# Kernel tuning notes

Hardware: AMD Instinct MI355X
Metric: run time of the kernel (lower is better)

Reference implementation:

```python
import jax, jax.numpy as jnp
import numpy as np

N_NODES = 50000
N_EDGES = 800000
D_IN = 128
D_HID = 128
N_CLASSES = 40


def gcn_conv(h, src, dst, W, b, n_nodes):
    """GCNConv: out = D^{-1/2} (A + I) D^{-1/2} (h @ W) + b, with self-loops."""
    h = h @ W  # [N, F_out]
    loop = jnp.arange(n_nodes, dtype=src.dtype)
    s = jnp.concatenate([src, loop])  # [E + N]
    d = jnp.concatenate([dst, loop])
    deg = jax.ops.segment_sum(jnp.ones_like(d, dtype=h.dtype), d, num_segments=n_nodes)
    dinv = jax.lax.rsqrt(jnp.maximum(deg, 1.0))  # deg >= 1 due to self-loops
    norm = dinv[s] * dinv[d]  # [E + N]
    msgs = h[s] * norm[:, None]  # gather: [E + N, F_out]
    out = jax.ops.segment_sum(msgs, d, num_segments=n_nodes)  # scatter-add
    return out + b


def setup_inputs() -> dict:
    key = jax.random.key(0)
    ks = jax.random.split(key, 12)
    x = jax.random.normal(ks[0], (N_NODES, D_IN), dtype=jnp.float32)
    edge_index = jax.random.randint(ks[1], (2, N_EDGES), 0, N_NODES, dtype=jnp.int64)
    def lin(k, fi, fo):
        s = 1.0 / np.sqrt(fi)
        return jax.random.uniform(k, (fi, fo), jnp.float32, -s, s)
    W_pre = lin(ks[2], D_IN, D_HID)
    b_pre = jnp.zeros((D_HID,), jnp.float32)
    W1 = lin(ks[3], D_HID, D_HID)
    b1 = jnp.zeros((D_HID,), jnp.float32)
    W2 = lin(ks[4], D_HID, D_HID)
    b2 = jnp.zeros((D_HID,), jnp.float32)
    W_post = lin(ks[5], D_HID, N_CLASSES)
    b_post = jnp.zeros((N_CLASSES,), jnp.float32)
    return {"x": x, "edge_index": edge_index, "W_pre": W_pre, "b_pre": b_pre,
            "W1": W1, "b1": b1, "W2": W2, "b2": b2,
            "W_post": W_post, "b_post": b_post}


def reference(x, edge_index, W_pre, b_pre, W1, b1, W2, b2, W_post, b_post):
    src, dst = edge_index[0], edge_index[1]
    n = x.shape[0]
    h = x @ W_pre + b_pre                      # pre-process MLP (Linear)
    h = jax.nn.relu(gcn_conv(h, src, dst, W1, b1, n))   # conv1 + act1
    h = jax.nn.relu(gcn_conv(h, src, dst, W2, b2, n))   # conv2 + act2
    return h @ W_post + b_post                 # post-process MLP (Linear)
```

## Files before the change

kernel.cpp:

```cpp
#include <hip/hip_runtime.h>

#define D 128

typedef short bfrag __attribute__((ext_vector_type(8)));
typedef float f32x4 __attribute__((ext_vector_type(4)));
typedef unsigned uint32;

__device__ inline unsigned short bf16_rne(float x) {
    unsigned u = __float_as_uint(x);
    return (unsigned short)((u + 0x7FFFu + ((u >> 16) & 1u)) >> 16);
}
__device__ inline float bf16_to_f(unsigned short h) {
    return __uint_as_float(((unsigned)h) << 16);
}
__device__ inline unsigned split2p(float x) {
    unsigned short hi = bf16_rne(x);
    unsigned short lo = bf16_rne(x - bf16_to_f(hi));
    return (unsigned)hi | ((unsigned)lo << 16);
}

__device__ inline void unpair_r(uint4 q0, uint4 q1, bfrag& ah, bfrag& al) {
    union { uint32 u[4]; bfrag b; } H, L;
    H.u[0] = __builtin_amdgcn_perm(q0.y, q0.x, 0x05040100u);
    H.u[1] = __builtin_amdgcn_perm(q0.w, q0.z, 0x05040100u);
    H.u[2] = __builtin_amdgcn_perm(q1.y, q1.x, 0x05040100u);
    H.u[3] = __builtin_amdgcn_perm(q1.w, q1.z, 0x05040100u);
    L.u[0] = __builtin_amdgcn_perm(q0.y, q0.x, 0x07060302u);
    L.u[1] = __builtin_amdgcn_perm(q0.w, q0.z, 0x07060302u);
    L.u[2] = __builtin_amdgcn_perm(q1.y, q1.x, 0x07060302u);
    L.u[3] = __builtin_amdgcn_perm(q1.w, q1.z, 0x07060302u);
    ah = H.b;
    al = L.b;
}

__device__ inline void split8_r(uint4 q0, uint4 q1, bfrag& ah, bfrag& al) {
    float v[8] = {__uint_as_float(q0.x), __uint_as_float(q0.y), __uint_as_float(q0.z), __uint_as_float(q0.w),
                  __uint_as_float(q1.x), __uint_as_float(q1.y), __uint_as_float(q1.z), __uint_as_float(q1.w)};
    union { unsigned short us[8]; bfrag b; } H, L;
    #pragma unroll
    for (int i = 0; i < 8; i++) {
        unsigned pr = split2p(v[i]);
        H.us[i] = (unsigned short)pr;
        L.us[i] = (unsigned short)(pr >> 16);
    }
    ah = H.b;
    al = L.b;
}

__global__ __launch_bounds__(256) void deg_raw(const unsigned* __restrict__ raw, int* __restrict__ deg,
                                               int* __restrict__ gmode, int E) {
    __shared__ int smode;
    int p0 = blockIdx.x * 1024;
    if (threadIdx.x < 64) {
        int p = p0 + threadIdx.x * 16;
        unsigned v = (p < E) ? raw[2 * p + 1] : 0u;
        unsigned long long any = __ballot(v != 0u);
        if (threadIdx.x == 0) smode = (any != 0ull) ? 1 : 0;
    }
    __syncthreads();
    int m = smode;
    if (blockIdx.x == 0 && threadIdx.x == 0) *gmode = m;
    int pend = min(p0 + 1024, E);
    for (int p = p0 + threadIdx.x; p < pend; p += 256) {
        int d = m ? (int)raw[E + p] : (int)((const unsigned long long*)raw)[E + p];
        atomicAdd(&deg[d], 1);
    }
}

__global__ __launch_bounds__(256) void rank_block(const int* __restrict__ deg, float* __restrict__ dinv,
                                                  int* __restrict__ local_rank, int* __restrict__ hist_blk, int N) {
    __shared__ int h[256];
    int t = threadIdx.x;
    h[t] = 0;
    __syncthreads();
    int i = blockIdx.x * 256 + t;
    if (i < N) {
        int d = deg[i];
        dinv[i] = 1.0f / sqrtf((float)(d + 1));
        int b = min(d, 255);
        local_rank[i] = atomicAdd(&h[b], 1);
    }
    __syncthreads();
    hist_blk[blockIdx.x * 256 + t] = h[t];
}

__global__ __launch_bounds__(256) void scan_blocks(int* __restrict__ hist_blk, int* __restrict__ binbase,
                                                   int* __restrict__ ebase, int nblk) {
    int b = threadIdx.x;
    int sum = 0;
    int k = 0;
    for (; k + 8 <= nblk; k += 8) {
        int v[8];
        #pragma unroll
        for (int u = 0; u < 8; u++) v[u] = hist_blk[(k + u) * 256 + b];
        #pragma unroll
        for (int u = 0; u < 8; u++) { hist_blk[(k + u) * 256 + b] = sum; sum += v[u]; }
    }
    for (; k < nblk; k++) {
        int v = hist_blk[k * 256 + b];
        hist_blk[k * 256 + b] = sum;
        sum += v;
    }
    __shared__ int s[256], s2[256];
    int c = sum, e = sum * b;
    s[b] = c; s2[b] = e;
    __syncthreads();
    for (int off = 1; off < 256; off <<= 1) {
        int a0 = (b >= off) ? s[b - off] : 0;
        int a1 = (b >= off) ? s2[b - off] : 0;
        __syncthreads();
        s[b] += a0; s2[b] += a1;
        __syncthreads();
    }
    binbase[b] = s[b] - c;
    ebase[b] = s2[b] - e;
}

__global__ __launch_bounds__(256) void emit_perm(const int* __restrict__ deg, const float* __restrict__ dinv,
                                                 const int* __restrict__ local_rank, const int* __restrict__ hist_blk,
                                                 const int* __restrict__ binbase, const int* __restrict__ ebase,
                                                 int* __restrict__ tailcur, int* __restrict__ rowbeg,
                                                 int* __restrict__ cursor, uint4* __restrict__ meta, int N) {
    int i = blockIdx.x * 256 + threadIdx.x;
    if (i >= N) return;
    int d = deg[i];
    int b = min(d, 255);
    int rib = hist_blk[blockIdx.x * 256 + b] + local_rank[i];
    int pos = binbase[b] + rib;
    int rb = (b < 255) ? (ebase[b] + rib * b) : (ebase[255] + atomicAdd(tailcur, d));
    rowbeg[i] = rb;
    cursor[i] = 0;
    meta[pos] = make_uint4((unsigned)rb, (unsigned)d, __float_as_uint(dinv[i]), (unsigned)i);
}

__global__ __launch_bounds__(256) void fill_csr_raw(const unsigned* __restrict__ raw, const int* __restrict__ gmode,
                                                    const int* __restrict__ rowbeg, int* __restrict__ cursor,
                                                    unsigned short* __restrict__ csr16, int E) {
    int e = blockIdx.x * 256 + threadIdx.x;
    if (e >= E) return;
    int m = *gmode;
    int d = m ? (int)raw[E + e] : (int)((const unsigned long long*)raw)[E + e];
    int s = m ? (int)raw[e]     : (int)((const unsigned long long*)raw)[e];
    int pos = atomicAdd(&cursor[d], 1);
    csr16[rowbeg[d] + pos] = (unsigned short)s;
}

__global__ __launch_bounds__(256) void prep_w_all(const float* __restrict__ Wpre, const float* __restrict__ W1,
                                                  const float* __restrict__ W2, const float* __restrict__ Wpost,
                                                  unsigned short* __restrict__ preh, unsigned short* __restrict__ prel,
                                                  unsigned short* __restrict__ w1h, unsigned short* __restrict__ w1l,
                                                  unsigned short* __restrict__ w2h, unsigned short* __restrict__ w2l,
                                                  unsigned short* __restrict__ poh, unsigned short* __restrict__ pol) {
    int i = blockIdx.x * 256 + threadIdx.x;
    const float* W; unsigned short *wh, *wl; int idx, ncols;
    if (i < 16384)      { W = Wpre;  wh = preh; wl = prel; idx = i;         ncols = 128; }
    else if (i < 32768) { W = W1;    wh = w1h;  wl = w1l;  idx = i - 16384; ncols = 128; }
    else if (i < 49152) { W = W2;    wh = w2h;  wl = w2l;  idx = i - 32768; ncols = 128; }
    else if (i < 55296) { W = Wpost; wh = poh;  wl = pol;  idx = i - 49152; ncols = 40;  }
    else return;
    int n = idx >> 7, k = idx & 127;
    float v = (n < ncols) ? W[k * ncols + n] : 0.f;
    unsigned p = split2p(v);
    wh[idx] = (unsigned short)p;
    wl[idx] = (unsigned short)(p >> 16);
}

template<int NTILES, int EPI, int AFMT, int NW>
__global__ __launch_bounds__(NW * 64) void gemm_mfma(const void* __restrict__ Ap,
                                                     const unsigned short* __restrict__ Wth,
                                                     const unsigned short* __restrict__ Wtl,
                                                     const float* __restrict__ bias,
                                                     const float* __restrict__ dinv,
                                                     float* __restrict__ Cf,
                                                     uint32* __restrict__ Pout,
                                                     int nStrips, int N, int outW) {
    int wave = threadIdx.x >> 6;
    int lane = threadIdx.x & 63;
    int l15 = lane & 15, lg = lane >> 4;
    int so, colbase;
    if (NW == 8) { so = wave >> 1; colbase = (wave & 1) * 64; }
    else         { so = wave;      colbase = 0; }
    size_t chunkStride = (size_t)nStrips * 256;

    bfrag wh[4][NTILES], wl[4][NTILES];
    #pragma unroll
    for (int ks = 0; ks < 4; ks++)
        #pragma unroll
        for (int nt = 0; nt < NTILES; nt++) {
            size_t off = (size_t)(colbase + nt * 16 + l15) * D + ks * 32 + lg * 8;
            wh[ks][nt] = *(const bfrag*)(Wth + off);
            wl[ks][nt] = *(const bfrag*)(Wtl + off);
        }

    const int stride = gridDim.x * 4;
    int strip = blockIdx.x * 4 + so;
    if (strip >= nStrips) return;

    uint4 cur[8];
    auto loadraw = [&](int s, uint4* r) {
        int arow = min(s * 16 + l15, N - 1);
        const uint4* p = (const uint4*)Ap + (size_t)arow * 32 + lg * 2;
        #pragma unroll
        for (int ks = 0; ks < 4; ks++) {
            r[2 * ks]     = p[ks * 8];
            r[2 * ks + 1] = p[ks * 8 + 1];
        }
    };

    loadraw(strip, cur);
    while (true) {
        int next = strip + stride;
        bool has_next = next < nStrips;
        uint4 nxt[8];
        if (has_next) loadraw(next, nxt);

        bfrag ah[4], al[4];
        #pragma unroll
        for (int ks = 0; ks < 4; ks++) {
            if (AFMT == 0) unpair_r(cur[2 * ks], cur[2 * ks + 1], ah[ks], al[ks]);
            else           split8_r(cur[2 * ks], cur[2 * ks + 1], ah[ks], al[ks]);
        }
        f32x4 acc[NTILES];
        #pragma unroll
        for (int nt = 0; nt < NTILES; nt++) acc[nt] = (f32x4){0.f, 0.f, 0.f, 0.f};
        #pragma unroll
        for (int ks = 0; ks < 4; ks++) {
            #pragma unroll
            for (int nt = 0; nt < NTILES; nt++)
                acc[nt] = __builtin_amdgcn_mfma_f32_16x16x32_bf16(ah[ks], wh[ks][nt], acc[nt], 0, 0, 0);
            #pragma unroll
            for (int nt = 0; nt < NTILES; nt++)
                acc[nt] = __builtin_amdgcn_mfma_f32_16x16x32_bf16(ah[ks], wl[ks][nt], acc[nt], 0, 0, 0);
            #pragma unroll
            for (int nt = 0; nt < NTILES; nt++)
                acc[nt] = __builtin_amdgcn_mfma_f32_16x16x32_bf16(al[ks], wh[ks][nt], acc[nt], 0, 0, 0);
        }

        int row0 = strip * 16;
        float dv[4];
        if (EPI == 0) {
            #pragma unroll
            for (int r = 0; r < 4; r++) {
                int row = row0 + lg * 4 + r;
                dv[r] = (row < N) ? dinv[row] : 0.f;
            }
        }
        #pragma unroll
        for (int nt = 0; nt < NTILES; nt++) {
            int col = colbase + nt * 16 + l15;
            #pragma unroll
            for (int r = 0; r < 4; r++) {
                int row = row0 + lg * 4 + r;
                if (row >= N) continue;
                float v = acc[nt][r];
                if (EPI == 0) {
                    Cf[(size_t)(col >> 4) * chunkStride + (size_t)row * 16 + (col & 15)] = v * dv[r];
                } else if (EPI == 1) {
                    Pout[(size_t)row * D + col] = split2p(v + bias[col]);
                } else {
                    if (col < outW) Cf[(size_t)row * outW + col] = v + bias[col];
                }
            }
        }
        if (!has_next) break;
        #pragma unroll
        for (int i = 0; i < 8; i++) cur[i] = nxt[i];
        strip = next;
    }
}

__global__ __launch_bounds__(256) void gather_xcd(const unsigned short* __restrict__ csr16,
                                                  const uint4* __restrict__ meta,
                                                  const float* __restrict__ t_c, const float* __restrict__ bias,
                                                  uint32* __restrict__ Pout, int N, int nStrips) {
    int chunk = blockIdx.x & 7;
    int k = (blockIdx.x >> 3) * 16 + (threadIdx.x >> 4);
    if (k >= N) return;
    uint4 m = meta[k];
    int beg = (int)m.x;
    int end = beg + (int)m.y;
    float di = __uint_as_float(m.z);
    int node = (int)m.w;
    int w = (threadIdx.x >> 2) & 3;
    int c = threadIdx.x & 3;
    const float* tc = t_c + (size_t)chunk * nStrips * 256 + c * 4;
    float4 a0 = make_float4(0.f, 0.f, 0.f, 0.f);
    float4 a1 = make_float4(0.f, 0.f, 0.f, 0.f);
    int j = beg + w;
    for (; j + 12 < end; j += 16) {
        int o0 = csr16[j];
        int o1 = csr16[j + 4];
        int o2 = csr16[j + 8];
        int o3 = csr16[j + 12];
        float4 v0 = *(const float4*)(tc + ((size_t)o0 << 4));
        float4 v1 = *(const float4*)(tc + ((size_t)o1 << 4));
        float4 v2 = *(const float4*)(tc + ((size_t)o2 << 4));
        float4 v3 = *(const float4*)(tc + ((size_t)o3 << 4));
        a0.x += v0.x; a0.y += v0.y; a0.z += v0.z; a0.w += v0.w;
        a1.x += v1.x; a1.y += v1.y; a1.z += v1.z; a1.w += v1.w;
        a0.x += v2.x; a0.y += v2.y; a0.z += v2.z; a0.w += v2.w;
        a1.x += v3.x; a1.y += v3.y; a1.z += v3.z; a1.w += v3.w;
    }
    for (; j < end; j += 4) {
        int o0 = csr16[j];
        float4 v0 = *(const float4*)(tc + ((size_t)o0 << 4));
        a0.x += v0.x; a0.y += v0.y; a0.z += v0.z; a0.w += v0.w;
    }
    a0.x += a1.x; a0.y += a1.y; a0.z += a1.z; a0.w += a1.w;
    a0.x += __shfl_xor(a0.x, 4); a0.y += __shfl_xor(a0.y, 4);
    a0.z += __shfl_xor(a0.z, 4); a0.w += __shfl_xor(a0.w, 4);
    a0.x += __shfl_xor(a0.x, 8); a0.y += __shfl_xor(a0.y, 8);
    a0.z += __shfl_xor(a0.z, 8); a0.w += __shfl_xor(a0.w, 8);
    if (w != 0) return;
    float4 tv = *(const float4*)(tc + (size_t)node * 16);
    int col0 = chunk * 16 + c * 4;
    float4 b = *((const float4*)bias + (col0 >> 2));
    float4 r;
    r.x = fmaxf(fmaf(di, a0.x + tv.x, b.x), 0.f);
    r.y = fmaxf(fmaf(di, a0.y + tv.y, b.y), 0.f);
    r.z = fmaxf(fmaf(di, a0.z + tv.z, b.z), 0.f);
    r.w = fmaxf(fmaf(di, a0.w + tv.w, b.w), 0.f);
    uint4 p;
    p.x = split2p(r.x); p.y = split2p(r.y); p.z = split2p(r.z); p.w = split2p(r.w);
    *(uint4*)(Pout + (size_t)node * D + col0) = p;
}

extern "C" void kernel_launch(void* const* d_in, const int* in_sizes, int n_in,
                              void* d_out, int out_size, void* d_ws, size_t ws_size,
                              hipStream_t stream) {
    const float* x      = (const float*)d_in[0];
    const unsigned* edges = (const unsigned*)d_in[1];
    const float* W_pre  = (const float*)d_in[2];
    const float* b_pre  = (const float*)d_in[3];
    const float* W1     = (const float*)d_in[4];
    const float* b1     = (const float*)d_in[5];
    const float* W2     = (const float*)d_in[6];
    const float* b2     = (const float*)d_in[7];
    const float* W_post = (const float*)d_in[8];
    const float* b_post = (const float*)d_in[9];
    float* out = (float*)d_out;

    const int N = in_sizes[0] / D;
    const int E = in_sizes[1] / 2;
    const int nStrips = (N + 15) / 16;
    const int Npad = nStrips * 16;
    const int nBlk = (N + 255) / 256;

    char* ws = (char*)d_ws;
    size_t off = 0;
    auto alloc = [&](size_t bytes) { void* p = ws + off; off += (bytes + 255) & ~(size_t)255; return p; };
    uint32* pairA = (uint32*)alloc((size_t)Npad * D * 4);
    uint32* pairB = (uint32*)alloc((size_t)Npad * D * 4);
    float*  bufT  = (float*)alloc((size_t)Npad * D * 4);
    float*  dinv    = (float*)alloc((size_t)N * 4);
    int*    deg     = (int*)alloc((size_t)N * 4);
    int*    rowbeg  = (int*)alloc((size_t)N * 4);
    unsigned short* csr16 = (unsigned short*)alloc((size_t)E * 2);
    uint4*  meta    = (uint4*)alloc((size_t)N * 16);
    unsigned short* wpre_h  = (unsigned short*)alloc(128 * 128 * 2);
    unsigned short* wpre_l  = (unsigned short*)alloc(128 * 128 * 2);
    unsigned short* w1_h    = (unsigned short*)alloc(128 * 128 * 2);
    unsigned short* w1_l    = (unsigned short*)alloc(128 * 128 * 2);
    unsigned short* w2_h    = (unsigned short*)alloc(128 * 128 * 2);
    unsigned short* w2_l    = (unsigned short*)alloc(128 * 128 * 2);
    unsigned short* wpost_h = (unsigned short*)alloc(48 * 128 * 2);
    unsigned short* wpost_l = (unsigned short*)alloc(48 * 128 * 2);

    {
        char* t = (char*)bufT;
        size_t toff = 0;
        auto talloc = [&](size_t bytes) { void* p = t + toff; toff += (bytes + 255) & ~(size_t)255; return p; };
        int* cursor     = (int*)talloc((size_t)N * 4);
        int* local_rank = (int*)talloc((size_t)N * 4);
        int* hist_blk   = (int*)talloc((size_t)nBlk * 256 * 4);
        int* mode2      = (int*)talloc(256);
        int* binbase    = (int*)talloc(1024);
        int* ebase      = (int*)talloc(1024);
        int* gmode = mode2;
        int* tailcur = mode2 + 1;

        (void)hipMemsetAsync(mode2, 0, 8, stream);
        (void)hipMemsetAsync(deg, 0, (size_t)N * 4, stream);
        deg_raw<<<(E + 1023) / 1024, 256, 0, stream>>>(edges, deg, gmode, E);
        rank_block<<<nBlk, 256, 0, stream>>>(deg, dinv, local_rank, hist_blk, N);
        scan_blocks<<<1, 256, 0, stream>>>(hist_blk, binbase, ebase, nBlk);
        emit_perm<<<nBlk, 256, 0, stream>>>(deg, dinv, local_rank, hist_blk, binbase, ebase,
                                            tailcur, rowbeg, cursor, meta, N);
        fill_csr_raw<<<(E + 255) / 256, 256, 0, stream>>>(edges, gmode, rowbeg, cursor, csr16, E);
    }

    prep_w_all<<<216, 256, 0, stream>>>(W_pre, W1, W2, W_post,
                                        wpre_h, wpre_l, w1_h, w1_l, w2_h, w2_l, wpost_h, wpost_l);

    const int nGatherBlocks = ((N + 15) / 16) * 8;

    gemm_mfma<4, 1, 1, 8><<<196, 512, 0, stream>>>(x, wpre_h, wpre_l, b_pre, nullptr, nullptr, pairB, nStrips, N, D);

    gemm_mfma<4, 0, 0, 8><<<196, 512, 0, stream>>>(pairB, w1_h, w1_l, nullptr, dinv, bufT, nullptr, nStrips, N, D);
    gather_xcd<<<nGatherBlocks, 256, 0, stream>>>(csr16, meta, bufT, b1, pairA, N, nStrips);

    gemm_mfma<4, 0, 0, 8><<<196, 512, 0, stream>>>(pairA, w2_h, w2_l, nullptr, dinv, bufT, nullptr, nStrips, N, D);
    gather_xcd<<<nGatherBlocks, 256, 0, stream>>>(csr16, meta, bufT, b2, pairB, N, nStrips);

    gemm_mfma<3, 2, 0, 4><<<196, 256, 0, stream>>>(pairB, wpost_h, wpost_l, b_post, nullptr, out, nullptr, nStrips, N, 40);
}
```

Baseline: 306.0 us.

## Pad CSR rows to multiples of four with sentinel zero rows for vector gather

Each CSR row's length is rounded up to a multiple of four. Padding slots are filled with a sentinel node index that points at zeroed extra rows appended to each feature chunk. The gather kernel can then load four indices with one ushort4 read, drop its remainder loop, and accumulate into four independent registers. The GEMM grid also grows from 196 to 256 blocks. In exchange the kernel adds sentinel initialisation work, a larger CSR buffer, and some wasted gathers of the zero row.

```diff
diff --git a/kernel.cpp b/kernel.cpp
--- a/kernel.cpp
+++ b/kernel.cpp
@@ -48,8 +48,11 @@
 }
 
 __global__ __launch_bounds__(256) void deg_raw(const unsigned* __restrict__ raw, int* __restrict__ deg,
-                                               int* __restrict__ gmode, int E) {
+                                               int* __restrict__ gmode, unsigned short* __restrict__ csr16,
+                                               float* __restrict__ t_c, int E, int N, int csrCap4, int nRows) {
     __shared__ int smode;
+    int gid = blockIdx.x * 256 + threadIdx.x;
+    int gstride = gridDim.x * 256;
     int p0 = blockIdx.x * 1024;
     if (threadIdx.x < 64) {
         int p = p0 + threadIdx.x * 16;
@@ -60,6 +63,15 @@
     __syncthreads();
     int m = smode;
     if (blockIdx.x == 0 && threadIdx.x == 0) *gmode = m;
+    unsigned short sent = (unsigned short)N;
+    ushort4 s4 = make_ushort4(sent, sent, sent, sent);
+    for (int i = gid; i < csrCap4; i += gstride) ((ushort4*)csr16)[i] = s4;
+    int nSentF4 = 8 * (nRows - N) * 4;
+    for (int i = gid; i < nSentF4; i += gstride) {
+        int chunk = i / ((nRows - N) * 4);
+        int rem = i % ((nRows - N) * 4);
+        ((float4*)(t_c + (size_t)chunk * nRows * 16 + (size_t)N * 16))[rem] = make_float4(0.f, 0.f, 0.f, 0.f);
+    }
     int pend = min(p0 + 1024, E);
     for (int p = p0 + threadIdx.x; p < pend; p += 256) {
         int d = m ? (int)raw[E + p] : (int)((const unsigned long long*)raw)[E + p];
@@ -102,7 +114,8 @@
         sum += v;
     }
     __shared__ int s[256], s2[256];
-    int c = sum, e = sum * b;
+    int bp = (b + 3) & ~3;
+    int c = sum, e = sum * bp;
     s[b] = c; s2[b] = e;
     __syncthreads();
     for (int off = 1; off < 256; off <<= 1) {
@@ -125,12 +138,13 @@
     if (i >= N) return;
     int d = deg[i];
     int b = min(d, 255);
+    int dp = (d + 3) & ~3;
     int rib = hist_blk[blockIdx.x * 256 + b] + local_rank[i];
     int pos = binbase[b] + rib;
-    int rb = (b < 255) ? (ebase[b] + rib * b) : (ebase[255] + atomicAdd(tailcur, d));
+    int rb = (b < 255) ? (ebase[b] + rib * ((b + 3) & ~3)) : (ebase[255] + atomicAdd(tailcur, dp));
     rowbeg[i] = rb;
     cursor[i] = 0;
-    meta[pos] = make_uint4((unsigned)rb, (unsigned)d, __float_as_uint(dinv[i]), (unsigned)i);
+    meta[pos] = make_uint4((unsigned)rb, (unsigned)dp, __float_as_uint(dinv[i]), (unsigned)i);
 }
 
 __global__ __launch_bounds__(256) void fill_csr_raw(const unsigned* __restrict__ raw, const int* __restrict__ gmode,
@@ -173,14 +187,14 @@
                                                      const float* __restrict__ dinv,
                                                      float* __restrict__ Cf,
                                                      uint32* __restrict__ Pout,
-                                                     int nStrips, int N, int outW) {
+                                                     int nStrips, int N, int outW, int nRows) {
     int wave = threadIdx.x >> 6;
     int lane = threadIdx.x & 63;
     int l15 = lane & 15, lg = lane >> 4;
     int so, colbase;
     if (NW == 8) { so = wave >> 1; colbase = (wave & 1) * 64; }
     else         { so = wave;      colbase = 0; }
-    size_t chunkStride = (size_t)nStrips * 256;
+    size_t chunkStride = (size_t)nRows * 16;
 
     bfrag wh[4][NTILES], wl[4][NTILES];
     #pragma unroll
@@ -272,41 +286,37 @@
 __global__ __launch_bounds__(256) void gather_xcd(const unsigned short* __restrict__ csr16,
                                                   const uint4* __restrict__ meta,
                                                   const float* __restrict__ t_c, const float* __restrict__ bias,
-                                                  uint32* __restrict__ Pout, int N, int nStrips) {
+                                                  uint32* __restrict__ Pout, int N, int nRows) {
     int chunk = blockIdx.x & 7;
     int k = (blockIdx.x >> 3) * 16 + (threadIdx.x >> 4);
     if (k >= N) return;
     uint4 m = meta[k];
     int beg = (int)m.x;
-    int end = beg + (int)m.y;
+    int degp = (int)m.y;
     float di = __uint_as_float(m.z);
     int node = (int)m.w;
     int w = (threadIdx.x >> 2) & 3;
     int c = threadIdx.x & 3;
-    const float* tc = t_c + (size_t)chunk * nStrips * 256 + c * 4;
+    const float* tc = t_c + (size_t)chunk * nRows * 16 + c * 4;
     float4 a0 = make_float4(0.f, 0.f, 0.f, 0.f);
     float4 a1 = make_float4(0.f, 0.f, 0.f, 0.f);
-    int j = beg + w;
-    for (; j + 12 < end; j += 16) {
-        int o0 = csr16[j];
-        int o1 = csr16[j + 4];
-        int o2 = csr16[j + 8];
-        int o3 = csr16[j + 12];
-        float4 v0 = *(const float4*)(tc + ((size_t)o0 << 4));
-        float4 v1 = *(const float4*)(tc + ((size_t)o1 << 4));
-        float4 v2 = *(const float4*)(tc + ((size_t)o2 << 4));
-        float4 v3 = *(const float4*)(tc + ((size_t)o3 << 4));
+    float4 a2 = make_float4(0.f, 0.f, 0.f, 0.f);
+    float4 a3 = make_float4(0.f, 0.f, 0.f, 0.f);
+    int end = beg + degp;
+    for (int j = beg + 4 * w; j < end; j += 16) {
+        ushort4 o = *(const ushort4*)(csr16 + j);
+        float4 v0 = *(const float4*)(tc + ((size_t)o.x << 4));
+        float4 v1 = *(const float4*)(tc + ((size_t)o.y << 4));
+        float4 v2 = *(const float4*)(tc + ((size_t)o.z << 4));
+        float4 v3 = *(const float4*)(tc + ((size_t)o.w << 4));
         a0.x += v0.x; a0.y += v0.y; a0.z += v0.z; a0.w += v0.w;
         a1.x += v1.x; a1.y += v1.y; a1.z += v1.z; a1.w += v1.w;
-        a0.x += v2.x; a0.y += v2.y; a0.z += v2.z; a0.w += v2.w;
-        a1.x += v3.x; a1.y += v3.y; a1.z += v3.z; a1.w += v3.w;
-    }
-    for (; j < end; j += 4) {
-        int o0 = csr16[j];
-        float4 v0 = *(const float4*)(tc + ((size_t)o0 << 4));
-        a0.x += v0.x; a0.y += v0.y; a0.z += v0.z; a0.w += v0.w;
+        a2.x += v2.x; a2.y += v2.y; a2.z += v2.z; a2.w += v2.w;
+        a3.x += v3.x; a3.y += v3.y; a3.z += v3.z; a3.w += v3.w;
     }
     a0.x += a1.x; a0.y += a1.y; a0.z += a1.z; a0.w += a1.w;
+    a2.x += a3.x; a2.y += a3.y; a2.z += a3.z; a2.w += a3.w;
+    a0.x += a2.x; a0.y += a2.y; a0.z += a2.z; a0.w += a2.w;
     a0.x += __shfl_xor(a0.x, 4); a0.y += __shfl_xor(a0.y, 4);
     a0.z += __shfl_xor(a0.z, 4); a0.w += __shfl_xor(a0.w, 4);
     a0.x += __shfl_xor(a0.x, 8); a0.y += __shfl_xor(a0.y, 8);
@@ -344,18 +354,20 @@
     const int E = in_sizes[1] / 2;
     const int nStrips = (N + 15) / 16;
     const int Npad = nStrips * 16;
+    const int nRows = Npad + 16;
     const int nBlk = (N + 255) / 256;
+    const int csrCap = (E + 4 * N + 255) & ~255;
 
     char* ws = (char*)d_ws;
     size_t off = 0;
     auto alloc = [&](size_t bytes) { void* p = ws + off; off += (bytes + 255) & ~(size_t)255; return p; };
     uint32* pairA = (uint32*)alloc((size_t)Npad * D * 4);
     uint32* pairB = (uint32*)alloc((size_t)Npad * D * 4);
-    float*  bufT  = (float*)alloc((size_t)Npad * D * 4);
+    float*  bufT  = (float*)alloc((size_t)8 * nRows * 16 * 4);
     float*  dinv    = (float*)alloc((size_t)N * 4);
     int*    deg     = (int*)alloc((size_t)N * 4);
     int*    rowbeg  = (int*)alloc((size_t)N * 4);
-    unsigned short* csr16 = (unsigned short*)alloc((size_t)E * 2);
+    unsigned short* csr16 = (unsigned short*)alloc((size_t)csrCap * 2);
     uint4*  meta    = (uint4*)alloc((size_t)N * 16);
     unsigned short* wpre_h  = (unsigned short*)alloc(128 * 128 * 2);
     unsigned short* wpre_l  = (unsigned short*)alloc(128 * 128 * 2);
@@ -381,7 +393,7 @@
 
         (void)hipMemsetAsync(mode2, 0, 8, stream);
         (void)hipMemsetAsync(deg, 0, (size_t)N * 4, stream);
-        deg_raw<<<(E + 1023) / 1024, 256, 0, stream>>>(edges, deg, gmode, E);
+        deg_raw<<<(E + 1023) / 1024, 256, 0, stream>>>(edges, deg, gmode, csr16, bufT, E, N, csrCap / 4, nRows);
         rank_block<<<nBlk, 256, 0, stream>>>(deg, dinv, local_rank, hist_blk, N);
         scan_blocks<<<1, 256, 0, stream>>>(hist_blk, binbase, ebase, nBlk);
         emit_perm<<<nBlk, 256, 0, stream>>>(deg, dinv, local_rank, hist_blk, binbase, ebase,
@@ -393,14 +405,15 @@
                                         wpre_h, wpre_l, w1_h, w1_l, w2_h, w2_l, wpost_h, wpost_l);
 
     const int nGatherBlocks = ((N + 15) / 16) * 8;
-
-    gemm_mfma<4, 1, 1, 8><<<196, 512, 0, stream>>>(x, wpre_h, wpre_l, b_pre, nullptr, nullptr, pairB, nStrips, N, D);
-
-    gemm_mfma<4, 0, 0, 8><<<196, 512, 0, stream>>>(pairB, w1_h, w1_l, nullptr, dinv, bufT, nullptr, nStrips, N, D);
-    gather_xcd<<<nGatherBlocks, 256, 0, stream>>>(csr16, meta, bufT, b1, pairA, N, nStrips);
-
-    gemm_mfma<4, 0, 0, 8><<<196, 512, 0, stream>>>(pairA, w2_h, w2_l, nullptr, dinv, bufT, nullptr, nStrips, N, D);
-    gather_xcd<<<nGatherBlocks, 256, 0, stream>>>(csr16, meta, bufT, b2, pairB, N, nStrips);
-
-    gemm_mfma<3, 2, 0, 4><<<196, 256, 0, stream>>>(pairB, wpost_h, wpost_l, b_post, nullptr, out, nullptr, nStrips, N, 40);
-}
+    const int gemmGrid = 256;
+
+    gemm_mfma<4, 1, 1, 8><<<gemmGrid, 512, 0, stream>>>(x, wpre_h, wpre_l, b_pre, nullptr, nullptr, pairB, nStrips, N, D, nRows);
+
+    gemm_mfma<4, 0, 0, 8><<<gemmGrid, 512, 0, stream>>>(pairB, w1_h, w1_l, nullptr, dinv, bufT, nullptr, nStrips, N, D, nRows);
+    gather_xcd<<<nGatherBlocks, 256, 0, stream>>>(csr16, meta, bufT, b1, pairA, N, nRows);
+
+    gemm_mfma<4, 0, 0, 8><<<gemmGrid, 512, 0, stream>>>(pairA, w2_h, w2_l, nullptr, dinv, bufT, nullptr, nStrips, N, D, nRows);
+    gather_xcd<<<nGatherBlocks, 256, 0, stream>>>(csr16, meta, bufT, b2, pairB, N, nRows);
+
+    gemm_mfma<3, 2, 0, 4><<<gemmGrid, 256, 0, stream>>>(pairB, wpost_h, wpost_l, b_post, nullptr, out, nullptr, nStrips, N, 40, nRows);
+}
```

Measured after the change: 297.6 us. 1.03x faster.
